# Performance work log

Hardware: AMD Instinct MI355X
Metric: run time of the kernel (lower is better)

## Reference

```python
import jax, jax.numpy as jnp
import numpy as np

# Clockwork RNN config (mirrors global args in the original script)
N1, N2, N3 = 16, 8, 8          # len(args.x1/x2/x3)
MULT = 8
DX = N1 + N2 + N3               # 32
D1, D2, D3 = N1*MULT, N2*MULT, N3*MULT  # 128, 64, 64
DH1 = DX * MULT                 # 256
DH2 = 512
DY = 4
T = 192
B = 512
R2, R3 = 2, 4                   # args.x2_rate, args.x3_rate


def _schedule_masks():
    # feat[j]: which input features are consumed at step j (zeroing a feature
    # is equivalent to slicing the matching rows of w_x).
    # blk[j]: which hidden units are updated at step j (others keep old value).
    feat = np.zeros((T, DX), np.float32)
    blk = np.zeros((T, DH1), np.bool_)
    for j in range(T):
        if (j + 1) % R2 == 0:
            if (j + 1) % R3 == 0:
                feat[j, :] = 1.0
                blk[j, :] = True
            else:
                feat[j, :N1 + N2] = 1.0
                blk[j, :D1 + D2] = True
        else:
            feat[j, :N1] = 1.0
            blk[j, :D1] = True
    return jnp.asarray(feat), jnp.asarray(blk)


def setup_inputs() -> dict:
    key = jax.random.key(0)
    ks = jax.random.split(key, 8)
    std = 1.0 / np.sqrt(DH1)
    u = lambda k, shape, s: jax.random.uniform(k, shape, jnp.float32, -s, s)
    return {
        "x": jax.random.normal(ks[0], (B, T, DX), jnp.float32),
        "w_x": u(ks[1], (DY, DX, DH1), std),
        "w_h": u(ks[2], (DY, DH1, DH1), std),
        "b": u(ks[3], (DY, DH1), std),
        "W1": u(ks[4], (DY, DH1, DH2), 1.0 / np.sqrt(DH1)),
        "b1": u(ks[5], (DY, DH2), 1.0 / np.sqrt(DH1)),
        "W2": u(ks[6], (DY, DH2), 1.0 / np.sqrt(DH2)),
        "b2": u(ks[7], (DY,), 1.0 / np.sqrt(DH2)),
    }


def reference(x, w_x, w_h, b, W1, b1, W2, b2):
    feat, blk = _schedule_masks()

    def step(h, inp):
        xj, fm, bm = inp              # xj:[B,DX] fm:[DX] bm:[DH1]
        xin = xj * fm                 # masked features == sliced w_x rows
        cand = jnp.tanh(
            jnp.einsum("bx,yxd->byd", xin, w_x)
            + jnp.einsum("byd,yde->bye", h, w_h)
            + b
        )                             # [B,DY,DH1]
        h = jnp.where(bm, cand, h)    # only scheduled blocks update
        return h, None

    h0 = jnp.zeros((x.shape[0], DY, DH1), x.dtype)
    hT, _ = jax.lax.scan(step, h0, (jnp.swapaxes(x, 0, 1), feat, blk))
    hid = jax.nn.relu(jnp.einsum("byd,ydh->byh", hT, W1) + b1)
    y = jnp.einsum("byh,yh->by", hid, W2) + b2   # [B,DY]
    return y
```

## Files before the change

kernel.cpp:

```cpp
#include <hip/hip_runtime.h>
#include <math.h>


#define TT    192
#define DXX   32
#define DH1   256
#define DH2   512
#define NY    4
#define ROWS8 8
#define PADK  264

typedef _Float16 f16x8 __attribute__((ext_vector_type(8)));
typedef __attribute__((ext_vector_type(4))) float f32x4;
typedef __attribute__((ext_vector_type(2))) int   i32x2;
typedef __attribute__((ext_vector_type(4))) int   i32x4;

template<int N> struct IC { static constexpr int v = N; };

__device__ __forceinline__ unsigned pkrtz(float a, float b) {
    unsigned d;
    asm("v_cvt_pkrtz_f16_f32 %0, %1, %2" : "=v"(d) : "v"(a), "v"(b));
    return d;
}
__device__ __forceinline__ unsigned short f16bits(_Float16 h) {
    union { _Float16 f; unsigned short u; } c; c.f = h; return c.u;
}
__device__ __forceinline__ float fast_tanh(float v) {
    float t = __builtin_amdgcn_exp2f(v * 2.885390081777927f);
    return fmaf(-2.f, __builtin_amdgcn_rcpf(t + 1.f), 1.f);
}

__global__ __launch_bounds__(512, 2) void cwrnn_mfma12(
    const float* __restrict__ x,
    const float* __restrict__ w_x,
    const float* __restrict__ w_h,
    const float* __restrict__ bias,
    const float* __restrict__ W1,
    const float* __restrict__ b1,
    const float* __restrict__ W2,
    const float* __restrict__ b2,
    float* __restrict__ out)
{
    __shared__ _Float16 hb[2][ROWS8 * PADK];
    __shared__ float red[8][ROWS8];
    __shared__ float scratch[DXX * DH1];

    const int t    = threadIdx.x;
    const int lane = t & 63;
    const int w    = t >> 6;
    const int r    = lane & 15;
    const int rb   = r & 7;
    const int q    = lane >> 4;
    const int y    = blockIdx.x & 3;
    const int b0   = (blockIdx.x >> 2) * ROWS8;

    const float* wx_g = w_x + (size_t)y * DXX * DH1;
    const float* wh_g = w_h + (size_t)y * DH1 * DH1;

    for (int i = t; i < ROWS8 * PADK; i += 512) hb[0][i] = (_Float16)0.f;

    f16x8 wxf[2];
    for (int i = t * 4; i < DXX * DH1; i += 2048)
        *(f32x4*)&scratch[i] = *(const f32x4*)&wx_g[i];
    __syncthreads();
    #pragma unroll
    for (int m = 0; m < 2; ++m) {
        f16x8 vh;
        #pragma unroll
        for (int jj = 0; jj < 8; ++jj)
            vh[jj] = (_Float16)scratch[(q * 8 + jj) * DH1 + ((m * 8 + w) << 4) + r];
        wxf[m] = vh;
    }
    __syncthreads();

    f16x8 whf[8][2];
    #pragma unroll
    for (int kt = 0; kt < 8; ++kt) {
        for (int i = t * 4; i < 32 * DH1; i += 2048)
            *(f32x4*)&scratch[i] = *(const f32x4*)&wh_g[kt * 32 * DH1 + i];
        __syncthreads();
        #pragma unroll
        for (int m = 0; m < 2; ++m) {
            f16x8 vh;
            #pragma unroll
            for (int jj = 0; jj < 8; ++jj)
                vh[jj] = (_Float16)scratch[(q * 8 + jj) * DH1 + ((m * 8 + w) << 4) + r];
            whf[kt][m] = vh;
        }
        __syncthreads();
    }

    f32x4 bias4[2];
    #pragma unroll
    for (int m = 0; m < 2; ++m)
        #pragma unroll
        for (int rr = 0; rr < 4; ++rr)
            bias4[m][rr] = bias[y * DH1 + ((m * 8 + w) << 4) + q * 4 + rr];

    const _Float16* hrd[2] = { &hb[0][rb * PADK] + q * 8,
                               &hb[1][rb * PADK] + q * 8 };
    const int tile_off = ((r < 8) ? w : 8 + w) << 4;
    _Float16* hws[2] = { &hb[0][rb * PADK + tile_off + q * 4],
                         &hb[1][rb * PADK + tile_off + q * 4] };

    const float* xrow = x + (size_t)(b0 + rb) * TT * DXX + q * 8;
    f32x4 cxa = *(const f32x4*)&xrow[0];
    f32x4 cxb = *(const f32x4*)&xrow[4];

    auto body = [&](int j, auto SC, int cur) {
        constexpr int S  = SC.v;
        constexpr int NF = (S == 0) ? 16 : (S == 1) ? 24 : 32;
        const bool m1act = (S == 2) || (S == 1 && w < 4);

        const int jn = (j + 1 < TT) ? j + 1 : j;
        const f32x4 pxa = *(const f32x4*)&xrow[jn * DXX];
        const f32x4 pxb = *(const f32x4*)&xrow[jn * DXX + 4];

        i32x2 old1;
        if (!m1act) old1 = *(const i32x2*)(hws[cur]);

        f16x8 xf;
        if (q * 8 < NF) {
            union { i32x4 i; f16x8 h; } ux;
            ux.i = (i32x4){ (int)pkrtz(cxa[0], cxa[1]), (int)pkrtz(cxa[2], cxa[3]),
                            (int)pkrtz(cxb[0], cxb[1]), (int)pkrtz(cxb[2], cxb[3]) };
            xf = ux.h;
        } else {
            xf = (f16x8)(_Float16)0.f;
        }

        const _Float16* hp = hrd[cur];

        f32x4 c0 = bias4[0], c1 = {0,0,0,0}, c2 = {0,0,0,0};
        f32x4 d0 = bias4[1], d1 = {0,0,0,0}, d2 = {0,0,0,0};

        __builtin_amdgcn_s_setprio(1);
        #pragma unroll
        for (int kt = 0; kt < 8; ++kt) {
            const f16x8 hv = *(const f16x8*)(hp + kt * 32);
            if ((kt % 3) == 0)
                c0 = __builtin_amdgcn_mfma_f32_16x16x32_f16(whf[kt][0], hv, c0, 0, 0, 0);
            else if ((kt % 3) == 1)
                c1 = __builtin_amdgcn_mfma_f32_16x16x32_f16(whf[kt][0], hv, c1, 0, 0, 0);
            else
                c2 = __builtin_amdgcn_mfma_f32_16x16x32_f16(whf[kt][0], hv, c2, 0, 0, 0);
            if (m1act) {
                if ((kt % 3) == 0)
                    d0 = __builtin_amdgcn_mfma_f32_16x16x32_f16(whf[kt][1], hv, d0, 0, 0, 0);
                else if ((kt % 3) == 1)
                    d1 = __builtin_amdgcn_mfma_f32_16x16x32_f16(whf[kt][1], hv, d1, 0, 0, 0);
                else
                    d2 = __builtin_amdgcn_mfma_f32_16x16x32_f16(whf[kt][1], hv, d2, 0, 0, 0);
            }
        }
        c2 = __builtin_amdgcn_mfma_f32_16x16x32_f16(wxf[0], xf, c2, 0, 0, 0);
        if (m1act)
            d2 = __builtin_amdgcn_mfma_f32_16x16x32_f16(wxf[1], xf, d2, 0, 0, 0);
        __builtin_amdgcn_s_setprio(0);

        {
            const f32x4 s0 = (c0 + c1) + c2;
            f32x4 sel;
            if (m1act) {
                const f32x4 s1 = (d0 + d1) + d2;
                sel[0] = (r < 8) ? s0[0] : s1[0];
                sel[1] = (r < 8) ? s0[1] : s1[1];
                sel[2] = (r < 8) ? s0[2] : s1[2];
                sel[3] = (r < 8) ? s0[3] : s1[3];
            } else {
                sel = s0;
            }
            const unsigned short h0 = f16bits((_Float16)fast_tanh(sel[0]));
            const unsigned short h1 = f16bits((_Float16)fast_tanh(sel[1]));
            const unsigned short h2 = f16bits((_Float16)fast_tanh(sel[2]));
            const unsigned short h3 = f16bits((_Float16)fast_tanh(sel[3]));
            i32x2 wv = (i32x2){ (int)(h0 | ((unsigned)h1 << 16)),
                                (int)(h2 | ((unsigned)h3 << 16)) };
            if (!m1act && r >= 8) wv = old1;
            *(i32x2*)(hws[cur ^ 1]) = wv;
        }
        __syncthreads();
        cxa = pxa; cxb = pxb;
    };

    for (int j = 0; j < TT; j += 4) {
        body(j + 0, IC<0>{}, 0);
        body(j + 1, IC<1>{}, 1);
        body(j + 2, IC<0>{}, 0);
        body(j + 3, IC<2>{}, 1);
    }

    float* hT = scratch;
    for (int i = t; i < DH1 * ROWS8; i += 512) {
        const int row = i & 7, k = i >> 3;
        hT[k * ROWS8 + row] = (float)hb[0][row * PADK + k];
    }
    __syncthreads();

    const float* W1_g = W1 + (size_t)y * DH1 * DH2;
    float a0[8];
    #pragma unroll
    for (int m = 0; m < 8; ++m) a0[m] = 0.f;
    for (int k = 0; k < DH1; ++k) {
        const float wv = W1_g[(size_t)k * DH2 + t];
        const f32x4 hA = *(const f32x4*)&hT[k * ROWS8];
        const f32x4 hB = *(const f32x4*)&hT[k * ROWS8 + 4];
        a0[0] += hA[0] * wv; a0[1] += hA[1] * wv;
        a0[2] += hA[2] * wv; a0[3] += hA[3] * wv;
        a0[4] += hB[0] * wv; a0[5] += hB[1] * wv;
        a0[6] += hB[2] * wv; a0[7] += hB[3] * wv;
    }
    {
        const float b1v = b1[y * DH2 + t];
        const float w2v = W2[y * DH2 + t];
        float p[8];
        #pragma unroll
        for (int m = 0; m < 8; ++m)
            p[m] = fmaxf(a0[m] + b1v, 0.f) * w2v;
        #pragma unroll
        for (int m = 0; m < 8; ++m) {
            float v = p[m];
            for (int off = 32; off > 0; off >>= 1) v += __shfl_down(v, off);
            if (lane == 0) red[w][m] = v;
        }
    }
    __syncthreads();
    if (t < ROWS8) {
        float s = b2[y];
        #pragma unroll
        for (int ww = 0; ww < 8; ++ww) s += red[ww][t];
        out[(size_t)(b0 + t) * NY + y] = s;
    }
}

extern "C" void kernel_launch(void* const* d_in, const int* in_sizes, int n_in,
                              void* d_out, int out_size, void* d_ws, size_t ws_size,
                              hipStream_t stream) {
    const float* x   = (const float*)d_in[0];
    const float* w_x = (const float*)d_in[1];
    const float* w_h = (const float*)d_in[2];
    const float* b   = (const float*)d_in[3];
    const float* W1  = (const float*)d_in[4];
    const float* b1  = (const float*)d_in[5];
    const float* W2  = (const float*)d_in[6];
    const float* b2  = (const float*)d_in[7];
    float* out = (float*)d_out;

    dim3 grid(256), block(512);
    hipLaunchKernelGGL(cwrnn_mfma12, grid, block, 0, stream,
                       x, w_x, w_h, b, W1, b1, W2, b2, out);
}
```

Baseline: 141.1 us.

## Preload packed fp16 inputs into shared memory and reorder MFMA chains

Before the recurrence, the block's whole x slice (8 rows × 192 steps) is converted to fp16 and stored in LDS, in a buffer unioned with the weight-staging scratch. Each step then reads x from LDS instead of issuing a global load per step. All eight hidden-state fragments are loaded up front, and the MFMA sequence is reordered so the c-chain runs fully before the d-chain. This removes global-memory latency from the serial recurrence but increases LDS use to about 96KB per block, which may limit occupancy.

After: 128.6 us. -8.8%, faster.

```diff
diff --git a/kernel.cpp b/kernel.cpp
--- a/kernel.cpp
+++ b/kernel.cpp
@@ -30,7 +30,7 @@
     return fmaf(-2.f, __builtin_amdgcn_rcpf(t + 1.f), 1.f);
 }
 
-__global__ __launch_bounds__(512, 2) void cwrnn_mfma12(
+__global__ __launch_bounds__(512, 2) void cwrnn_mfma13(
     const float* __restrict__ x,
     const float* __restrict__ w_x,
     const float* __restrict__ w_h,
@@ -43,7 +43,11 @@
 {
     __shared__ _Float16 hb[2][ROWS8 * PADK];
     __shared__ float red[8][ROWS8];
-    __shared__ float scratch[DXX * DH1];
+    __shared__ __align__(16) union Pool {
+        float scratch[DXX * DH1];
+        short xpk[TT * 256];
+    } pool;
+    __shared__ __align__(16) int xzero[4];
 
     const int t    = threadIdx.x;
     const int lane = t & 63;
@@ -58,17 +62,18 @@
     const float* wh_g = w_h + (size_t)y * DH1 * DH1;
 
     for (int i = t; i < ROWS8 * PADK; i += 512) hb[0][i] = (_Float16)0.f;
+    if (t < 4) xzero[t] = 0;
 
     f16x8 wxf[2];
     for (int i = t * 4; i < DXX * DH1; i += 2048)
-        *(f32x4*)&scratch[i] = *(const f32x4*)&wx_g[i];
+        *(f32x4*)&pool.scratch[i] = *(const f32x4*)&wx_g[i];
     __syncthreads();
     #pragma unroll
     for (int m = 0; m < 2; ++m) {
         f16x8 vh;
         #pragma unroll
         for (int jj = 0; jj < 8; ++jj)
-            vh[jj] = (_Float16)scratch[(q * 8 + jj) * DH1 + ((m * 8 + w) << 4) + r];
+            vh[jj] = (_Float16)pool.scratch[(q * 8 + jj) * DH1 + ((m * 8 + w) << 4) + r];
         wxf[m] = vh;
     }
     __syncthreads();
@@ -77,17 +82,31 @@
     #pragma unroll
     for (int kt = 0; kt < 8; ++kt) {
         for (int i = t * 4; i < 32 * DH1; i += 2048)
-            *(f32x4*)&scratch[i] = *(const f32x4*)&wh_g[kt * 32 * DH1 + i];
+            *(f32x4*)&pool.scratch[i] = *(const f32x4*)&wh_g[kt * 32 * DH1 + i];
         __syncthreads();
         #pragma unroll
         for (int m = 0; m < 2; ++m) {
             f16x8 vh;
             #pragma unroll
             for (int jj = 0; jj < 8; ++jj)
-                vh[jj] = (_Float16)scratch[(q * 8 + jj) * DH1 + ((m * 8 + w) << 4) + r];
+                vh[jj] = (_Float16)pool.scratch[(q * 8 + jj) * DH1 + ((m * 8 + w) << 4) + r];
             whf[kt][m] = vh;
         }
         __syncthreads();
+    }
+
+    for (int it = 0; it < 12; ++it) {
+        const int idx = t + it * 512;
+        const int rbz = idx / 768;
+        const int rem = idx - rbz * 768;
+        const int j   = rem >> 2;
+        const int qq  = idx & 3;
+        const float* xp = x + ((size_t)(b0 + rbz) * TT + j) * DXX + qq * 8;
+        const f32x4 a = *(const f32x4*)xp;
+        const f32x4 b = *(const f32x4*)(xp + 4);
+        *(i32x4*)&pool.xpk[j * 256 + rbz * 32 + qq * 8] =
+            (i32x4){ (int)pkrtz(a[0], a[1]), (int)pkrtz(a[2], a[3]),
+                     (int)pkrtz(b[0], b[1]), (int)pkrtz(b[2], b[3]) };
     }
 
     f32x4 bias4[2];
@@ -102,60 +121,55 @@
     const int tile_off = ((r < 8) ? w : 8 + w) << 4;
     _Float16* hws[2] = { &hb[0][rb * PADK + tile_off + q * 4],
                          &hb[1][rb * PADK + tile_off + q * 4] };
-
-    const float* xrow = x + (size_t)(b0 + rb) * TT * DXX + q * 8;
-    f32x4 cxa = *(const f32x4*)&xrow[0];
-    f32x4 cxb = *(const f32x4*)&xrow[4];
-
-    auto body = [&](int j, auto SC, int cur) {
+    const short* xcur = pool.xpk + rb * 32 + q * 8;
+    const short* xz   = (const short*)xzero;
+
+    __syncthreads();
+
+    auto body = [&](int jmod, auto SC, int cur) {
         constexpr int S  = SC.v;
         constexpr int NF = (S == 0) ? 16 : (S == 1) ? 24 : 32;
         const bool m1act = (S == 2) || (S == 1 && w < 4);
 
-        const int jn = (j + 1 < TT) ? j + 1 : j;
-        const f32x4 pxa = *(const f32x4*)&xrow[jn * DXX];
-        const f32x4 pxb = *(const f32x4*)&xrow[jn * DXX + 4];
-
         i32x2 old1;
         if (!m1act) old1 = *(const i32x2*)(hws[cur]);
 
-        f16x8 xf;
-        if (q * 8 < NF) {
-            union { i32x4 i; f16x8 h; } ux;
-            ux.i = (i32x4){ (int)pkrtz(cxa[0], cxa[1]), (int)pkrtz(cxa[2], cxa[3]),
-                            (int)pkrtz(cxb[0], cxb[1]), (int)pkrtz(cxb[2], cxb[3]) };
-            xf = ux.h;
-        } else {
-            xf = (f16x8)(_Float16)0.f;
-        }
-
         const _Float16* hp = hrd[cur];
+        f16x8 hv0 = *(const f16x8*)(hp + 0 * 32);
+        f16x8 hv1 = *(const f16x8*)(hp + 1 * 32);
+        f16x8 hv2 = *(const f16x8*)(hp + 2 * 32);
+        f16x8 hv3 = *(const f16x8*)(hp + 3 * 32);
+        f16x8 hv4 = *(const f16x8*)(hp + 4 * 32);
+        f16x8 hv5 = *(const f16x8*)(hp + 5 * 32);
+        f16x8 hv6 = *(const f16x8*)(hp + 6 * 32);
+        f16x8 hv7 = *(const f16x8*)(hp + 7 * 32);
+        const short* xptr = (q * 8 < NF) ? (xcur + jmod * 256) : xz;
+        const f16x8 xf = *(const f16x8*)xptr;
 
         f32x4 c0 = bias4[0], c1 = {0,0,0,0}, c2 = {0,0,0,0};
         f32x4 d0 = bias4[1], d1 = {0,0,0,0}, d2 = {0,0,0,0};
 
         __builtin_amdgcn_s_setprio(1);
-        #pragma unroll
-        for (int kt = 0; kt < 8; ++kt) {
-            const f16x8 hv = *(const f16x8*)(hp + kt * 32);
-            if ((kt % 3) == 0)
-                c0 = __builtin_amdgcn_mfma_f32_16x16x32_f16(whf[kt][0], hv, c0, 0, 0, 0);
-            else if ((kt % 3) == 1)
-                c1 = __builtin_amdgcn_mfma_f32_16x16x32_f16(whf[kt][0], hv, c1, 0, 0, 0);
-            else
-                c2 = __builtin_amdgcn_mfma_f32_16x16x32_f16(whf[kt][0], hv, c2, 0, 0, 0);
-            if (m1act) {
-                if ((kt % 3) == 0)
-                    d0 = __builtin_amdgcn_mfma_f32_16x16x32_f16(whf[kt][1], hv, d0, 0, 0, 0);
-                else if ((kt % 3) == 1)
-                    d1 = __builtin_amdgcn_mfma_f32_16x16x32_f16(whf[kt][1], hv, d1, 0, 0, 0);
-                else
-                    d2 = __builtin_amdgcn_mfma_f32_16x16x32_f16(whf[kt][1], hv, d2, 0, 0, 0);
-            }
-        }
-        c2 = __builtin_amdgcn_mfma_f32_16x16x32_f16(wxf[0], xf, c2, 0, 0, 0);
-        if (m1act)
-            d2 = __builtin_amdgcn_mfma_f32_16x16x32_f16(wxf[1], xf, d2, 0, 0, 0);
+        c0 = __builtin_amdgcn_mfma_f32_16x16x32_f16(whf[0][0], hv0, c0, 0, 0, 0);
+        c1 = __builtin_amdgcn_mfma_f32_16x16x32_f16(whf[1][0], hv1, c1, 0, 0, 0);
+        c2 = __builtin_amdgcn_mfma_f32_16x16x32_f16(whf[2][0], hv2, c2, 0, 0, 0);
+        c0 = __builtin_amdgcn_mfma_f32_16x16x32_f16(whf[3][0], hv3, c0, 0, 0, 0);
+        c1 = __builtin_amdgcn_mfma_f32_16x16x32_f16(whf[4][0], hv4, c1, 0, 0, 0);
+        c2 = __builtin_amdgcn_mfma_f32_16x16x32_f16(whf[5][0], hv5, c2, 0, 0, 0);
+        c0 = __builtin_amdgcn_mfma_f32_16x16x32_f16(whf[6][0], hv6, c0, 0, 0, 0);
+        c1 = __builtin_amdgcn_mfma_f32_16x16x32_f16(whf[7][0], hv7, c1, 0, 0, 0);
+        c2 = __builtin_amdgcn_mfma_f32_16x16x32_f16(wxf[0],    xf,  c2, 0, 0, 0);
+        if (m1act) {
+            d0 = __builtin_amdgcn_mfma_f32_16x16x32_f16(whf[0][1], hv0, d0, 0, 0, 0);
+            d1 = __builtin_amdgcn_mfma_f32_16x16x32_f16(whf[1][1], hv1, d1, 0, 0, 0);
+            d2 = __builtin_amdgcn_mfma_f32_16x16x32_f16(whf[2][1], hv2, d2, 0, 0, 0);
+            d0 = __builtin_amdgcn_mfma_f32_16x16x32_f16(whf[3][1], hv3, d0, 0, 0, 0);
+            d1 = __builtin_amdgcn_mfma_f32_16x16x32_f16(whf[4][1], hv4, d1, 0, 0, 0);
+            d2 = __builtin_amdgcn_mfma_f32_16x16x32_f16(whf[5][1], hv5, d2, 0, 0, 0);
+            d0 = __builtin_amdgcn_mfma_f32_16x16x32_f16(whf[6][1], hv6, d0, 0, 0, 0);
+            d1 = __builtin_amdgcn_mfma_f32_16x16x32_f16(whf[7][1], hv7, d1, 0, 0, 0);
+            d2 = __builtin_amdgcn_mfma_f32_16x16x32_f16(wxf[1],    xf,  d2, 0, 0, 0);
+        }
         __builtin_amdgcn_s_setprio(0);
 
         {
@@ -180,17 +194,18 @@
             *(i32x2*)(hws[cur ^ 1]) = wv;
         }
         __syncthreads();
-        cxa = pxa; cxb = pxb;
     };
 
     for (int j = 0; j < TT; j += 4) {
-        body(j + 0, IC<0>{}, 0);
-        body(j + 1, IC<1>{}, 1);
-        body(j + 2, IC<0>{}, 0);
-        body(j + 3, IC<2>{}, 1);
-    }
-
-    float* hT = scratch;
+        body(0, IC<0>{}, 0);
+        body(1, IC<1>{}, 1);
+        body(2, IC<0>{}, 0);
+        body(3, IC<2>{}, 1);
+        xcur += 1024;
+    }
+
+    __syncthreads();
+    float* hT = pool.scratch;
     for (int i = t; i < DH1 * ROWS8; i += 512) {
         const int row = i & 7, k = i >> 3;
         hT[k * ROWS8 + row] = (float)hb[0][row * PADK + k];
@@ -247,6 +262,6 @@
     float* out = (float*)d_out;
 
     dim3 grid(256), block(512);
-    hipLaunchKernelGGL(cwrnn_mfma12, grid, block, 0, stream,
+    hipLaunchKernelGGL(cwrnn_mfma13, grid, block, 0, stream,
                        x, w_x, w_h, b, W1, b1, W2, b2, out);
 }
```
